# Kernel optimization log

Measured on AMD Instinct MI355X. Metric: run time of the kernel, lower is better.

## Reference

```python
import math
import jax, jax.numpy as jnp
import numpy as np

D_MODEL = 1024
N_HEADS = 16
HEAD_DIM = 64          # block_size
NUM_RULES = 64
RANK = 8               # proj_rank = round(sqrt(head_dim)); also router_rank
SHARED_RANK = 32       # round(sqrt(d_model))
NUM_BLOCKS = 16        # min(in,out)//block_size = 1024//64; total_block_dim == d_model
B, S = 4, 1024
ROPE_BASE = 10000.0


def setup_inputs() -> dict:
    key = jax.random.key(0)
    ks = iter(jax.random.split(key, 32))
    def nrm(shape, s=0.02):
        return jax.random.normal(next(ks), shape, dtype=jnp.float32) * s
    inp = {
        "x": jax.random.normal(next(ks), (B, S, D_MODEL), dtype=jnp.float32),
        "target_rule_ids": jax.random.randint(next(ks), (B, S), 0, NUM_RULES),
    }
    for p in ("q", "k", "v", "o"):
        inp[p + "_si"] = nrm((D_MODEL, SHARED_RANK))
        inp[p + "_so"] = nrm((SHARED_RANK, D_MODEL))
        inp[p + "_ri"] = nrm((NUM_RULES, HEAD_DIM, RANK))
        inp[p + "_ro"] = nrm((NUM_RULES, RANK, HEAD_DIM))
        inp[p + "_lg"] = nrm((NUM_RULES, NUM_BLOCKS), 1.0 / math.sqrt(NUM_BLOCKS))
    inp["router_q"] = nrm((NUM_RULES, RANK))
    inp["router_k"] = nrm((NUM_RULES, RANK))
    return inp


def _rule_proj(x, rules, si, so, ri, ro, lg):
    """RuleAwareProjection.forward_rules_batched, de-permuted.

    The torch code argsorts tokens by rule, zero-pads per-rule buckets, runs
    bmm per rule and scatters back; mathematically that equals a per-token
    gather of the rule's low-rank adapter, which is what we compute here.
    x: [N, D_MODEL], rules: [N] int.
    """
    base = (x @ si) @ so                                  # shared low-rank path
    xb = x.reshape(-1, NUM_BLOCKS, HEAD_DIM)              # [N, nb, bs]
    h = jnp.einsum('nbs,nsr->nbr', xb, ri[rules])         # [N, nb, rank]
    a = jnp.einsum('nbr,nrt->nbt', h, ro[rules])          # [N, nb, bs]
    # temperature = 1/sqrt(num_blocks) => logits / temperature = logits*sqrt(nb)
    sel = jax.nn.softmax(lg[rules] * math.sqrt(NUM_BLOCKS), axis=-1)
    return base + (a * sel[:, :, None]).reshape(-1, D_MODEL)


def _rope(q, k):
    # q, k: [B, H, S, D]; interleaved-pair rotation, start_pos = 0.
    S_, D = q.shape[2], q.shape[3]
    pos = jnp.arange(S_, dtype=jnp.float32)[:, None]
    div = jnp.exp(jnp.arange(0, D, 2, dtype=jnp.float32) * (-math.log(ROPE_BASE) / D))
    f = pos * div                                         # [S, D/2]
    sin, cos = jnp.sin(f), jnp.cos(f)
    def rot(t):
        t1, t2 = t[..., 0::2], t[..., 1::2]
        return jnp.stack([t1 * cos - t2 * sin, t2 * cos + t1 * sin], axis=-1).reshape(t.shape)
    return rot(q), rot(k)


def reference(x, target_rule_ids,
              q_si, q_so, q_ri, q_ro, q_lg,
              k_si, k_so, k_ri, k_ro, k_lg,
              v_si, v_so, v_ri, v_ro, v_lg,
              o_si, o_so, o_ri, o_ro, o_lg,
              router_q, router_k):
    B_, S_, C = x.shape
    flat_x = x.reshape(-1, C)
    rules = target_rule_ids.reshape(-1)

    q = _rule_proj(flat_x, rules, q_si, q_so, q_ri, q_ro, q_lg)
    k = _rule_proj(flat_x, rules, k_si, k_so, k_ri, k_ro, k_lg)
    v = _rule_proj(flat_x, rules, v_si, v_so, v_ri, v_ro, v_lg)
    q = q.reshape(B_, S_, N_HEADS, HEAD_DIM).transpose(0, 2, 1, 3)
    k = k.reshape(B_, S_, N_HEADS, HEAD_DIM).transpose(0, 2, 1, 3)
    v = v.reshape(B_, S_, N_HEADS, HEAD_DIM).transpose(0, 2, 1, 3)
    q, k = _rope(q, k)

    # rule-routing sparse mask: cosine affinity between token rule embeddings
    rq = router_q[target_rule_ids]                        # [B, S, rank]
    rk = router_k[target_rule_ids]
    rqn = rq / jnp.maximum(jnp.linalg.norm(rq, axis=-1, keepdims=True), 1e-12)
    rkn = rk / jnp.maximum(jnp.linalg.norm(rk, axis=-1, keepdims=True), 1e-12)
    tau = 1.0 / math.log(max(math.e, RANK))
    aff = jnp.einsum('bqr,bkr->bqk', rqn, rkn) / tau       # [B, S, S]
    causal = jnp.tril(jnp.ones((S_, S_), dtype=bool))
    masked = jnp.where(causal[None], aff, -jnp.inf)
    top_k = max(2, int(math.sqrt(S_)))
    if S_ > top_k:
        thr = jax.lax.top_k(masked, top_k)[0][..., -1:]
        rule_mask = (masked >= thr) & causal[None]
    else:
        rule_mask = jnp.broadcast_to(causal[None], masked.shape)

    scores = jnp.einsum('bhqd,bhkd->bhqk', q, k) / math.sqrt(HEAD_DIM)
    scores = jnp.where(rule_mask[:, None], scores, -jnp.inf)
    attn = jax.nn.softmax(scores, axis=-1)
    out = jnp.einsum('bhqk,bhkd->bhqd', attn, v)
    out = out.transpose(0, 2, 1, 3).reshape(-1, C)
    out = _rule_proj(out, rules, o_si, o_so, o_ri, o_ro, o_lg)
    return out.reshape(B_, S_, C)
```

## Files before the change

kernel.cpp:

```cpp
#include <hip/hip_runtime.h>
#include <hip/hip_bf16.h>
#include <hip/hip_fp16.h>

#define D_MODEL 1024
#define N_HEADS 16
#define HEAD_DIM 64
#define NUM_RULES 64
#define RANK 8
#define SHARED_RANK 32
#define NUM_BLOCKS_ 16
#define BB 4
#define SS 1024
#define NTOK (BB*SS)
#define NGRP (NTOK/8)
#define NGRP4 (NTOK/4)

typedef __attribute__((ext_vector_type(8))) short bf16x8;
typedef __attribute__((ext_vector_type(4))) float f32x4;

__device__ __forceinline__ float bf2f(unsigned short u) {
  unsigned int i = ((unsigned int)u) << 16;
  float f;
  __builtin_memcpy(&f, &i, 4);
  return f;
}
__device__ __forceinline__ unsigned short f2bf(float f) {
  __hip_bfloat16 h = __float2bfloat16(f);
  unsigned short u;
  __builtin_memcpy(&u, &h, 2);
  return u;
}
__device__ __forceinline__ unsigned short f2h(float f) {
  __half h = __float2half(f);
  unsigned short u;
  __builtin_memcpy(&u, &h, 2);
  return u;
}
__device__ __forceinline__ float h2f(unsigned short u) {
  __half h;
  __builtin_memcpy(&h, &u, 2);
  return __half2float(h);
}
template<bool BF>
__device__ __forceinline__ float ldw(const void* p, size_t i) {
  if (BF) return bf2f(((const unsigned short*)p)[i]);
  else    return ((const float*)p)[i];
}

__global__ void detect_kernel(const unsigned short* __restrict__ x, int* __restrict__ flag) {
  const int lane = threadIdx.x;
  int good = 0;
  for (int i = 0; i < 4; i++) {
    unsigned short u = x[lane*4 + i];
    int e = (u >> 7) & 0xFF;
    good += (e == 0 || (e >= 100 && e <= 145)) ? 1 : 0;
  }
  for (int off = 32; off; off >>= 1) good += __shfl_xor(good, off);
  if (lane == 0) flag[0] = (good >= 224) ? 1 : 0;
}

template<bool BF>
__device__ __forceinline__ void precompute_body(
    const void* rq, const void* rk,
    const void* qlg, const void* klg, const void* vlg, const void* olg,
    float* __restrict__ M, float* __restrict__ sel)
{
  __shared__ float rqn[64][8], rkn[64][8];
  const int tid = threadIdx.x;
  if (tid < 64) {
    float v[8]; float s = 0.f;
    for (int i = 0; i < 8; i++) { v[i] = ldw<BF>(rq, tid*8+i); s += v[i]*v[i]; }
    float inv = 1.0f / fmaxf(sqrtf(s), 1e-12f);
    for (int i = 0; i < 8; i++) rqn[tid][i] = v[i]*inv;
  } else if (tid < 128) {
    int r = tid - 64;
    float v[8]; float s = 0.f;
    for (int i = 0; i < 8; i++) { v[i] = ldw<BF>(rk, r*8+i); s += v[i]*v[i]; }
    float inv = 1.0f / fmaxf(sqrtf(s), 1e-12f);
    for (int i = 0; i < 8; i++) rkn[r][i] = v[i]*inv;
  }
  __syncthreads();
  const float LN8 = 2.0794415416798357f;
  for (int idx = tid; idx < 64*64; idx += 256) {
    int i = idx >> 6, j = idx & 63;
    float d = 0.f;
    for (int t = 0; t < 8; t++) d += rqn[i][t]*rkn[j][t];
    M[idx] = d * LN8;
  }
  const void* lgs[4] = {qlg, klg, vlg, olg};
  {
    int r = tid & 63;
    const void* lg = lgs[tid >> 6];
    float e[NUM_BLOCKS_]; float mx = -1e30f;
    for (int b = 0; b < NUM_BLOCKS_; b++) {
      e[b] = ldw<BF>(lg, r*NUM_BLOCKS_ + b) * 4.0f;
      mx = fmaxf(mx, e[b]);
    }
    float s = 0.f;
    for (int b = 0; b < NUM_BLOCKS_; b++) { e[b] = expf(e[b]-mx); s += e[b]; }
    float inv = 1.0f/s;
    for (int b = 0; b < NUM_BLOCKS_; b++) sel[tid*NUM_BLOCKS_+b] = e[b]*inv;
  }
}

__global__ void precompute_kernel(
    const void* rq, const void* rk,
    const void* qlg, const void* klg, const void* vlg, const void* olg,
    float* M, float* sel, const int* __restrict__ flag)
{
  if (*flag) precompute_body<true >(rq, rk, qlg, klg, vlg, olg, M, sel);
  else       precompute_body<false>(rq, rk, qlg, klg, vlg, olg, M, sel);
}

__global__ __launch_bounds__(128) void prep_wb_kernel(
    const float* __restrict__ qsi, const float* __restrict__ ksi,
    const float* __restrict__ vsi, const float* __restrict__ osi,
    unsigned short* __restrict__ wh, unsigned short* __restrict__ wl,
    const int* __restrict__ flag)
{
  if (*flag) return;
  const int kt = blockIdx.x, p = blockIdx.y;
  const int tid = threadIdx.x, nt = tid >> 6, lane = tid & 63;
  const float* si = (p==0)?qsi:((p==1)?ksi:((p==2)?vsi:osi));
  const int col = nt*16 + (lane & 15);
  const int k0 = kt*32 + (lane >> 4)*8;
  size_t base = ((((size_t)p*32 + kt)*2 + nt)*64 + lane)*8;
  unsigned short h8[8], l8[8];
  #pragma unroll
  for (int j = 0; j < 8; j++) {
    float f = si[(size_t)(k0 + j)*SHARED_RANK + col];
    unsigned short hu = f2bf(f);
    h8[j] = hu;
    l8[j] = f2bf(f - bf2f(hu));
  }
  #pragma unroll
  for (int j = 0; j < 8; j++) { wh[base + j] = h8[j]; wl[base + j] = l8[j]; }
}

template<int NPROJ>
__device__ __forceinline__ void tt_mfma_body(
    const float* __restrict__ xin,
    const unsigned short* __restrict__ wh, const unsigned short* __restrict__ wl,
    int p0, float* __restrict__ ttg)
{
  const int NT = NPROJ*2;
  const int tile = blockIdx.x;
  const int tid = threadIdx.x, lane = tid & 63, w = tid >> 6;
  const int kq = lane >> 4;
  __shared__ float red[4][64][25];

  f32x4 acc[NT];
  #pragma unroll
  for (int i = 0; i < NT; i++) acc[i] = (f32x4){0.f,0.f,0.f,0.f};

  const float* xrow = xin + (size_t)(tile*16 + (lane & 15))*D_MODEL + kq*8;
  #pragma unroll 2
  for (int s = 0; s < 8; s++) {
    const int kt = w*8 + s;
    float4 a0 = *(const float4*)(xrow + kt*32);
    float4 a1 = *(const float4*)(xrow + kt*32 + 4);
    float av[8] = {a0.x,a0.y,a0.z,a0.w,a1.x,a1.y,a1.z,a1.w};
    bf16x8 ah, al;
    #pragma unroll
    for (int j = 0; j < 8; j++) {
      unsigned short hu = f2bf(av[j]);
      ah[j] = (short)hu;
      al[j] = (short)f2bf(av[j] - bf2f(hu));
    }
    #pragma unroll
    for (int p = 0; p < NPROJ; p++) {
      #pragma unroll
      for (int nt = 0; nt < 2; nt++) {
        size_t bidx = ((((size_t)(p0+p)*32 + kt)*2 + nt)*64 + lane)*8;
        bf16x8 bh = *(const bf16x8*)(wh + bidx);
        bf16x8 bl = *(const bf16x8*)(wl + bidx);
        f32x4 c = acc[p*2+nt];
        c = __builtin_amdgcn_mfma_f32_16x16x32_bf16(ah, bh, c, 0, 0, 0);
        c = __builtin_amdgcn_mfma_f32_16x16x32_bf16(al, bh, c, 0, 0, 0);
        c = __builtin_amdgcn_mfma_f32_16x16x32_bf16(ah, bl, c, 0, 0, 0);
        acc[p*2+nt] = c;
      }
    }
  }
  #pragma unroll
  for (int i = 0; i < NT; i++) {
    red[w][lane][i*4+0] = acc[i][0]; red[w][lane][i*4+1] = acc[i][1];
    red[w][lane][i*4+2] = acc[i][2]; red[w][lane][i*4+3] = acc[i][3];
  }
  __syncthreads();
  if (w == 0) {
    const int tok0 = tile*16 + (lane >> 4)*4;
    #pragma unroll
    for (int i = 0; i < NT; i++) {
      const int ys = i >> 1, jj = (i & 1)*16 + (lane & 15);
      #pragma unroll
      for (int r = 0; r < 4; r++) {
        float sum = red[0][lane][i*4+r] + red[1][lane][i*4+r]
                  + red[2][lane][i*4+r] + red[3][lane][i*4+r];
        ttg[((size_t)ys*NTOK + tok0 + r)*32 + jj] = sum;
      }
    }
  }
}

__global__ __launch_bounds__(256) void A_tt_mfma3(
    const float* __restrict__ xin,
    const unsigned short* __restrict__ wh, const unsigned short* __restrict__ wl,
    float* __restrict__ ttg, const int* __restrict__ flag)
{
  if (*flag) return;
  tt_mfma_body<3>(xin, wh, wl, 0, ttg);
}

__global__ __launch_bounds__(256) void A_tt_mfma1(
    const float* __restrict__ xin,
    const unsigned short* __restrict__ wh, const unsigned short* __restrict__ wl,
    float* __restrict__ ttg, const int* __restrict__ flag)
{
  if (*flag) return;
  tt_mfma_body<1>(xin, wh, wl, 3, ttg);
}

template<int NP>
__device__ __forceinline__ void hh_body(
    const float* __restrict__ xin, const int* __restrict__ rules,
    const float* __restrict__ ri0, const float* __restrict__ ri1,
    const float* __restrict__ ri2, float* __restrict__ hhg)
{
  const int g = blockIdx.x, n0 = g*8, tid = threadIdx.x;
  const int t = tid >> 5, blk = (tid >> 1) & 15, r0 = (tid & 1)*4;
  const int n = n0 + t;
  const int rule = rules[n];
  const float* xb = xin + (size_t)n*D_MODEL + blk*64;
  const float* wb[3];
  wb[0] = ri0 + (size_t)rule*512 + r0;
  if (NP > 1) {
    wb[1] = ri1 + (size_t)rule*512 + r0;
    wb[2] = ri2 + (size_t)rule*512 + r0;
  }
  float a[NP][4];
  #pragma unroll
  for (int p = 0; p < NP; p++) { a[p][0]=0.f; a[p][1]=0.f; a[p][2]=0.f; a[p][3]=0.f; }
  #pragma unroll 4
  for (int k4 = 0; k4 < 16; k4++) {
    float4 xv = *(const float4*)(xb + k4*4);
    #pragma unroll
    for (int q = 0; q < 4; q++) {
      const int k = k4*4 + q;
      float xq = (q==0)?xv.x:((q==1)?xv.y:((q==2)?xv.z:xv.w));
      #pragma unroll
      for (int p = 0; p < NP; p++) {
        float4 wv = *(const float4*)(wb[p] + (size_t)k*8);
        a[p][0] += xq*wv.x; a[p][1] += xq*wv.y; a[p][2] += xq*wv.z; a[p][3] += xq*wv.w;
      }
    }
  }
  #pragma unroll
  for (int p = 0; p < NP; p++) {
    float4 hv; hv.x=a[p][0]; hv.y=a[p][1]; hv.z=a[p][2]; hv.w=a[p][3];
    *(float4*)&hhg[((size_t)p*NTOK + n)*128 + blk*8 + r0] = hv;
  }
}

__global__ __launch_bounds__(256) void A_hh3_f32(
    const float* __restrict__ xin, const int* __restrict__ rules,
    const float* __restrict__ qri, const float* __restrict__ kri,
    const float* __restrict__ vri, float* __restrict__ hhg,
    const int* __restrict__ flag)
{
  if (*flag) return;
  hh_body<3>(xin, rules, qri, kri, vri, hhg);
}

__global__ __launch_bounds__(256) void A_hh1_f32(
    const float* __restrict__ xin, const int* __restrict__ rules,
    const float* __restrict__ ori, float* __restrict__ hhg,
    const int* __restrict__ flag)
{
  if (*flag) return;
  hh_body<1>(xin, rules, ori, ori, ori, hhg);
}

template<bool IN_BF, bool W_BF>
__device__ __forceinline__ void stageA_body(
    const void* __restrict__ xin, const int* __restrict__ rules,
    const void* __restrict__ si, const void* __restrict__ ri,
    float* __restrict__ ttg, float* __restrict__ hhg, int yslot)
{
  const int g = blockIdx.x, n0 = g*8, tid = threadIdx.x;
  __shared__ float xs[8][D_MODEL];
  __shared__ float tpart[8][32][9];
  __shared__ int rl[8];

  #pragma unroll
  for (int t = 0; t < 8; t++) {
    float4 f;
    if (IN_BF) {
      ushort4 u = ((const ushort4*)((const unsigned short*)xin + (size_t)(n0+t)*D_MODEL))[tid];
      f.x = bf2f(u.x); f.y = bf2f(u.y); f.z = bf2f(u.z); f.w = bf2f(u.w);
    } else {
      f = ((const float4*)xin)[(size_t)(n0+t)*(D_MODEL/4) + tid];
    }
    *(float4*)&xs[t][tid*4] = f;
  }
  if (tid < 8) rl[tid] = rules[n0 + tid];
  __syncthreads();

  {
    const int c = tid >> 5, j = tid & 31;
    float p[8];
    #pragma unroll
    for (int t = 0; t < 8; t++) p[t] = 0.f;
    #pragma unroll 4
    for (int d4 = 0; d4 < 32; d4++) {
      const int d = c*128 + d4*4;
      float w0 = ldw<W_BF>(si, (size_t)(d+0)*SHARED_RANK + j);
      float w1 = ldw<W_BF>(si, (size_t)(d+1)*SHARED_RANK + j);
      float w2 = ldw<W_BF>(si, (size_t)(d+2)*SHARED_RANK + j);
      float w3 = ldw<W_BF>(si, (size_t)(d+3)*SHARED_RANK + j);
      #pragma unroll
      for (int t = 0; t < 8; t++) {
        float4 xv = *(const float4*)&xs[t][d];
        p[t] += xv.x*w0 + xv.y*w1 + xv.z*w2 + xv.w*w3;
      }
    }
    #pragma unroll
    for (int t = 0; t < 8; t++) tpart[c][j][t] = p[t];
  }
  __syncthreads();

  {
    const int t = tid >> 5, j = tid & 31;
    float s = 0.f;
    #pragma unroll
    for (int c = 0; c < 8; c++) s += tpart[c][j][t];
    ttg[((size_t)yslot*NTOK + n0 + t)*32 + j] = s;
  }
  {
    const int t = tid >> 5, blk = (tid >> 1) & 15, r0 = (tid & 1)*4;
    const int rule = rl[t];
    float a0=0.f, a1=0.f, a2=0.f, a3=0.f;
    #pragma unroll 4
    for (int k4 = 0; k4 < 16; k4++) {
      const int kk = ((k4 + blk) & 15) * 4;
      float4 xv = *(const float4*)&xs[t][blk*64 + kk];
      #pragma unroll
      for (int q = 0; q < 4; q++) {
        const int k = kk + q;
        float w0,w1,w2,w3;
        if (W_BF) {
          ushort4 u = *(const ushort4*)((const unsigned short*)ri + (size_t)rule*512 + (size_t)k*8 + r0);
          w0=bf2f(u.x); w1=bf2f(u.y); w2=bf2f(u.z); w3=bf2f(u.w);
        } else {
          float4 u = *(const float4*)((const float*)ri + (size_t)rule*512 + (size_t)k*8 + r0);
          w0=u.x; w1=u.y; w2=u.z; w3=u.w;
        }
        float xq = (q==0)?xv.x:((q==1)?xv.y:((q==2)?xv.z:xv.w));
        a0 += xq*w0; a1 += xq*w1; a2 += xq*w2; a3 += xq*w3;
      }
    }
    float4 hv; hv.x=a0; hv.y=a1; hv.z=a2; hv.w=a3;
    *(float4*)&hhg[((size_t)yslot*NTOK + n0 + t)*128 + blk*8 + r0] = hv;
  }
}

__global__ __launch_bounds__(256) void A_qkv_bf16(
    const void* x, const int* rules,
    const void* qsi, const void* qri, const void* ksi, const void* kri,
    const void* vsi, const void* vri,
    float* ttg, float* hhg, const int* __restrict__ flag)
{
  if (!*flag) return;
  const int y = blockIdx.y;
  const void* si = (y==0)?qsi:((y==1)?ksi:vsi);
  const void* ri = (y==0)?qri:((y==1)?kri:vri);
  stageA_body<true,true>(x, rules, si, ri, ttg, hhg, y);
}

__global__ __launch_bounds__(256) void A_o_bf16(
    const void* ain, const int* rules, const void* osi, const void* ori,
    float* ttg, float* hhg, const int* __restrict__ flag)
{
  if (!*flag) return;
  stageA_body<false,true>(ain, rules, osi, ori, ttg, hhg, 0);
}

template<bool W_BF>
__device__ __forceinline__ void stageB_body(
    const float* __restrict__ ttg, const float* __restrict__ hhg,
    const int* __restrict__ rules,
    const void* __restrict__ so, const void* __restrict__ ro,
    const float* __restrict__ sel, void* __restrict__ out,
    int yslot, int do_rope, int out_bf)
{
  const int blk4 = blockIdx.x;
  const int n0 = blk4*4, tid = threadIdx.x;
  __shared__ float tt_lds[32][5];
  __shared__ float hh_lds[4][132];
  __shared__ int rl[4];

  if (tid < 128) {
    const int j = tid >> 2, t4 = tid & 3;
    tt_lds[j][t4] = ttg[((size_t)yslot*NTOK + n0 + t4)*32 + j];
  } else if (tid < 256 && (tid - 128) < 128) {
    const int i = tid - 128;
    const int t4 = i >> 5, c = (i*4) & 127;
    float4 hv = *(const float4*)&hhg[((size_t)yslot*NTOK + n0 + t4)*128 + c];
    *(float4*)&hh_lds[t4][c] = hv;
  }
  if (tid < 4) rl[tid] = rules[n0 + tid];
  __syncthreads();

  const int ch0 = tid*4;
  float a0[4], a1[4], a2[4], a3[4];
  #pragma unroll
  for (int t = 0; t < 4; t++) { a0[t]=0.f; a1[t]=0.f; a2[t]=0.f; a3[t]=0.f; }

  #pragma unroll 4
  for (int j = 0; j < 32; j++) {
    float w0, w1, w2, w3;
    if (W_BF) {
      ushort4 u = *(const ushort4*)((const unsigned short*)so + (size_t)j*D_MODEL + ch0);
      w0=bf2f(u.x); w1=bf2f(u.y); w2=bf2f(u.z); w3=bf2f(u.w);
    } else {
      float4 u = *(const float4*)((const float*)so + (size_t)j*D_MODEL + ch0);
      w0=u.x; w1=u.y; w2=u.z; w3=u.w;
    }
    #pragma unroll
    for (int t = 0; t < 4; t++) {
      float tv = tt_lds[j][t];
      a0[t] += tv*w0; a1[t] += tv*w1; a2[t] += tv*w2; a3[t] += tv*w3;
    }
  }

  const int blk = ch0 >> 6, tc = ch0 & 63;
  float inv0 = 0.f, inv1 = 0.f;
  if (do_rope) {
    inv0 = expf(-(float)tc     * (9.210340371976184f/64.0f));
    inv1 = expf(-(float)(tc+2) * (9.210340371976184f/64.0f));
  }
  #pragma unroll 2
  for (int t = 0; t < 4; t++) {
    const int rule = rl[t];
    float b0=0.f, b1=0.f, b2=0.f, b3=0.f;
    #pragma unroll
    for (int r = 0; r < 8; r++) {
      float w0,w1,w2,w3;
      if (W_BF) {
        ushort4 u = *(const ushort4*)((const unsigned short*)ro + (size_t)rule*512 + r*64 + tc);
        w0=bf2f(u.x); w1=bf2f(u.y); w2=bf2f(u.z); w3=bf2f(u.w);
      } else {
        float4 u = *(const float4*)((const float*)ro + (size_t)rule*512 + r*64 + tc);
        w0=u.x; w1=u.y; w2=u.z; w3=u.w;
      }
      float hv = hh_lds[t][blk*8 + r];
      b0 += hv*w0; b1 += hv*w1; b2 += hv*w2; b3 += hv*w3;
    }
    float sb = sel[rule*NUM_BLOCKS_ + blk];
    float e0 = a0[t] + b0*sb, o0 = a1[t] + b1*sb;
    float e1 = a2[t] + b2*sb, o1 = a3[t] + b3*sb;
    const int n = n0 + t;
    if (do_rope) {
      float spos = (float)(n & (SS-1));
      float sn0, cs0, sn1, cs1;
      sincosf(spos*inv0, &sn0, &cs0);
      sincosf(spos*inv1, &sn1, &cs1);
      float u0 = e0*cs0 - o0*sn0; o0 = o0*cs0 + e0*sn0; e0 = u0;
      float u1 = e1*cs1 - o1*sn1; o1 = o1*cs1 + e1*sn1; e1 = u1;
    }
    if (out_bf) {
      ushort4 uv; uv.x=f2bf(e0); uv.y=f2bf(o0); uv.z=f2bf(e1); uv.w=f2bf(o1);
      *(ushort4*)((unsigned short*)out + (size_t)n*D_MODEL + ch0) = uv;
    } else {
      float4 fv; fv.x=e0; fv.y=o0; fv.z=e1; fv.w=o1;
      *(float4*)((float*)out + (size_t)n*D_MODEL + ch0) = fv;
    }
  }
}

__global__ __launch_bounds__(256) void B_qkv(
    const float* ttg, const float* hhg, const int* rules,
    const void* qso, const void* qro, const void* kso, const void* kro,
    const void* vso, const void* vro,
    const float* sel, float* qb, unsigned short* kb, unsigned short* vb,
    const int* __restrict__ flag)
{
  const int y = blockIdx.y;
  const void* so = (y==0)?qso:((y==1)?kso:vso);
  const void* ro = (y==0)?qro:((y==1)?kro:vro);
  void* out = (y==0)?(void*)qb:((y==1)?(void*)kb:(void*)vb);
  if (*flag)
    stageB_body<true >(ttg, hhg, rules, so, ro, sel + y*1024, out, y, (y<2)?1:0, (y>=1)?1:0);
  else
    stageB_body<false>(ttg, hhg, rules, so, ro, sel + y*1024, out, y, (y<2)?1:0, (y>=1)?1:0);
}

__global__ __launch_bounds__(256) void B_o(
    const float* ttg, const float* hhg, const int* rules,
    const void* oso, const void* oro, const float* sel, void* out,
    const int* __restrict__ flag)
{
  if (*flag) stageB_body<true >(ttg, hhg, rules, oso, oro, sel, out, 0, 0, 1);
  else       stageB_body<false>(ttg, hhg, rules, oso, oro, sel, out, 0, 0, 0);
}

__global__ __launch_bounds__(64) void mask_kernel(
    const int* __restrict__ rules, const float* __restrict__ M,
    unsigned long long* __restrict__ am, unsigned int* __restrict__ rp)
{
  const int bid = blockIdx.x;
  const int b = bid >> 10, qi = bid & 1023;
  const int lane = threadIdx.x;
  __shared__ int rrow[SS];
  __shared__ float val[64];
  __shared__ int cnth[64];
  for (int i = lane; i < SS/4; i += 64)
    ((int4*)rrow)[i] = ((const int4*)(rules + b*SS))[i];
  cnth[lane] = 0;
  __syncthreads();
  if (qi < 16 && lane < 16) {
    unsigned v = 0;
    #pragma unroll
    for (int nt = 0; nt < 4; nt++)
      v |= ((unsigned)rrow[qi*64 + nt*16 + lane] & 0xffu) << (8*nt);
    rp[b*256 + qi*16 + lane] = v;
  }
  for (int k = lane; k <= qi; k += 64) atomicAdd(&cnth[rrow[k]], 1);
  const int qrule = rrow[qi];
  const float myv = M[qrule*64 + lane];
  val[lane] = myv;
  __syncthreads();
  const int c = cnth[lane];
  int A = 0;
  for (int r = 0; r < 64; r++) {
    int cr = __shfl(c, r);
    A += (val[r] > myv) ? cr : 0;
  }
  unsigned long long allowed = __ballot(A < 32);
  if (lane == 0) am[bid] = allowed;
}

__global__ __launch_bounds__(256) void vtrans_kernel(
    const unsigned short* __restrict__ vb, unsigned short* __restrict__ vt)
{
  const int st = blockIdx.x, h = blockIdx.y, b = blockIdx.z;
  __shared__ unsigned short t[64][72];
  const int tid = threadIdx.x;
  #pragma unroll
  for (int it = 0; it < 2; it++) {
    int i = tid + it*256;
    int r = i >> 3, c8 = (i & 7)*8;
    uint4 v = *(const uint4*)(vb + ((size_t)(b*SS + st*64 + r)*D_MODEL + h*HEAD_DIM + c8));
    t[c8+0][r] = (unsigned short)(v.x & 0xffffu);
    t[c8+1][r] = (unsigned short)(v.x >> 16);
    t[c8+2][r] = (unsigned short)(v.y & 0xffffu);
    t[c8+3][r] = (unsigned short)(v.y >> 16);
    t[c8+4][r] = (unsigned short)(v.z & 0xffffu);
    t[c8+5][r] = (unsigned short)(v.z >> 16);
    t[c8+6][r] = (unsigned short)(v.w & 0xffffu);
    t[c8+7][r] = (unsigned short)(v.w >> 16);
  }
  __syncthreads();
  #pragma unroll
  for (int it = 0; it < 2; it++) {
    int i = tid + it*256;
    int d = i >> 3, c8 = i & 7;
    uint4 o = *(const uint4*)&t[d][c8*8];
    *(uint4*)(vt + ((size_t)(b*N_HEADS + h)*HEAD_DIM + d)*SS + st*64 + c8*8) = o;
  }
}

__global__ __launch_bounds__(256, 4) void attn_mfma_kernel(
    const float* __restrict__ qb,
    const unsigned short* __restrict__ kb,
    const unsigned short* __restrict__ vtb,
    const unsigned int* __restrict__ rp,
    const unsigned long long* __restrict__ am,
    unsigned short* __restrict__ Obuf,
    float* __restrict__ mlbuf,
    float* outb)
{
  const int x = blockIdx.x, b = blockIdx.y, h = blockIdx.z;
  int qt, k0t, k1t, pidx;
  bool partial;
  if (x < 9) { qt = x; k0t = 0; k1t = qt; partial = false; pidx = 0; }
  else {
    const int j = x - 9, qti = j >> 1, s = j & 1;
    qt = 9 + qti; partial = true;
    pidx = ((b*N_HEADS + h)*7 + qti)*2 + s;
    if (s == 0) { k0t = 0; k1t = 7; } else { k0t = 8; k1t = qt; }
  }
  const int tid = threadIdx.x, lane = tid & 63, w = tid >> 6;
  __shared__ unsigned short Ks[64*64];
  __shared__ unsigned short Vs[64*64];
  __shared__ unsigned short Pl[4][16*64];

  const unsigned short* kbase = kb + (size_t)b*SS*D_MODEL + h*HEAD_DIM;
  const unsigned short* vbase = vtb + (size_t)(b*N_HEADS + h)*HEAD_DIM*SS;
  const unsigned int* rpb = rp + b*256;

  const int srow = tid >> 3;
  const int spos = tid & 7;
  const int kc0 = (srow*8      + (spos ^ (srow        & 7)))*8;
  const int kc1 = ((srow+32)*8 + (spos ^ ((srow+32)   & 7)))*8;
  unsigned short* pw = &Pl[w][0];

  const int qa = qt*64 + w*16 + (lane & 15);
  bf16x8 qfrag[2];
  {
    const float* qrow = qb + (size_t)(b*SS + qa)*D_MODEL + h*HEAD_DIM + (lane>>4)*8;
    #pragma unroll
    for (int kc = 0; kc < 2; kc++) {
      float4 f0 = *(const float4*)(qrow + kc*32);
      float4 f1 = *(const float4*)(qrow + kc*32 + 4);
      bf16x8 qv;
      qv[0] = (short)f2bf(f0.x*0.125f); qv[1] = (short)f2bf(f0.y*0.125f);
      qv[2] = (short)f2bf(f0.z*0.125f); qv[3] = (short)f2bf(f0.w*0.125f);
      qv[4] = (short)f2bf(f1.x*0.125f); qv[5] = (short)f2bf(f1.y*0.125f);
      qv[6] = (short)f2bf(f1.z*0.125f); qv[7] = (short)f2bf(f1.w*0.125f);
      qfrag[kc] = qv;
    }
  }
  int qg[4]; unsigned aqlo[4], aqhi[4];
  #pragma unroll
  for (int r = 0; r < 4; r++) {
    qg[r] = qt*64 + w*16 + (lane>>4)*4 + r;
    uint2 mm = *(const uint2*)(am + (size_t)b*SS + qg[r]);
    aqlo[r] = mm.x; aqhi[r] = mm.y;
  }
  f32x4 Oacc[4];
  #pragma unroll
  for (int nt = 0; nt < 4; nt++) Oacc[nt] = (f32x4){0.f,0.f,0.f,0.f};
  float lrun[4];
  #pragma unroll
  for (int r = 0; r < 4; r++) lrun[r] = 0.f;

  {
    const size_t koff0 = (size_t)k0t*64;
    uint4 k0 = *(const uint4*)(kbase + (koff0 + srow)*D_MODEL + spos*8);
    uint4 k1 = *(const uint4*)(kbase + (koff0 + srow + 32)*D_MODEL + spos*8);
    uint4 v0 = *(const uint4*)(vbase + (size_t)srow*SS + koff0 + spos*8);
    uint4 v1 = *(const uint4*)(vbase + (size_t)(srow+32)*SS + koff0 + spos*8);
    *(uint4*)&Ks[kc0] = k0; *(uint4*)&Ks[kc1] = k1;
    *(uint4*)&Vs[kc0] = v0; *(uint4*)&Vs[kc1] = v1;
  }
  __syncthreads();

  for (int kt = k0t; kt <= k1t; kt++) {
    const unsigned ru = rpb[kt*16 + (lane & 15)];
    uint4 nk0, nk1, nv0, nv1;
    if (kt < k1t) {
      const size_t koff = (size_t)(kt + 1)*64;
      nk0 = *(const uint4*)(kbase + (koff + srow)*D_MODEL + spos*8);
      nk1 = *(const uint4*)(kbase + (koff + srow + 32)*D_MODEL + spos*8);
      nv0 = *(const uint4*)(vbase + (size_t)srow*SS + koff + spos*8);
      nv1 = *(const uint4*)(vbase + (size_t)(srow+32)*SS + koff + spos*8);
    }

    f32x4 Sacc[4];
    __builtin_amdgcn_s_setprio(1);
    #pragma unroll
    for (int nt = 0; nt < 4; nt++) {
      const int key = nt*16 + (lane & 15);
      f32x4 c = (f32x4){0.f,0.f,0.f,0.f};
      #pragma unroll
      for (int kc = 0; kc < 2; kc++) {
        int off = (key*128 + kc*64 + (lane>>4)*16) ^ ((key & 7) << 4);
        bf16x8 kf = *(const bf16x8*)((const char*)Ks + off);
        c = __builtin_amdgcn_mfma_f32_16x16x32_bf16(qfrag[kc], kf, c, 0, 0, 0);
      }
      Sacc[nt] = c;
    }
    __builtin_amdgcn_s_setprio(0);

    const bool needc = (kt == qt);
    float sv[4][4];
    #pragma unroll
    for (int nt = 0; nt < 4; nt++) {
      const int k = kt*64 + nt*16 + (lane & 15);
      const unsigned rr = (ru >> (nt*8)) & 0xffu;
      const unsigned sh = rr & 31u;
      const bool hi = rr >= 32;
      #pragma unroll
      for (int r = 0; r < 4; r++) {
        unsigned bits = hi ? aqhi[r] : aqlo[r];
        bool ok = (((bits >> sh) & 1u) != 0u);
        if (needc) ok = ok && (k <= qg[r]);
        sv[nt][r] = ok ? Sacc[nt][r] : -3e38f;
      }
    }

    #pragma unroll
    for (int nt = 0; nt < 4; nt++) {
      #pragma unroll
      for (int r = 0; r < 4; r++) {
        float p = __expf(sv[nt][r]);
        lrun[r] += p;
        const int q = (lane>>4)*4 + r;
        int off = (q*128 + (nt*16 + (lane & 15))*2) ^ ((q & 7) << 4);
        *(unsigned short*)((char*)pw + off) = f2bf(p);
      }
    }

    __builtin_amdgcn_s_setprio(1);
    #pragma unroll
    for (int kc = 0; kc < 2; kc++) {
      const int qrow = lane & 15;
      int aoff = (qrow*128 + kc*64 + (lane>>4)*16) ^ ((qrow & 7) << 4);
      bf16x8 pa = *(const bf16x8*)((const char*)pw + aoff);
      #pragma unroll
      for (int nt = 0; nt < 4; nt++) {
        const int d = nt*16 + (lane & 15);
        int boff = (d*128 + kc*64 + (lane>>4)*16) ^ ((d & 7) << 4);
        bf16x8 vf = *(const bf16x8*)((const char*)Vs + boff);
        Oacc[nt] = __builtin_amdgcn_mfma_f32_16x16x32_bf16(pa, vf, Oacc[nt], 0, 0, 0);
      }
    }
    __builtin_amdgcn_s_setprio(0);
    __syncthreads();
    if (kt < k1t) {
      *(uint4*)&Ks[kc0] = nk0; *(uint4*)&Ks[kc1] = nk1;
      *(uint4*)&Vs[kc0] = nv0; *(uint4*)&Vs[kc1] = nv1;
      __syncthreads();
    }
  }

  #pragma unroll
  for (int off = 1; off < 16; off <<= 1) {
    #pragma unroll
    for (int r = 0; r < 4; r++) lrun[r] += __shfl_xor(lrun[r], off);
  }

  if (!partial) {
    float invl[4];
    #pragma unroll
    for (int r = 0; r < 4; r++) invl[r] = 1.0f / lrun[r];
    #pragma unroll
    for (int nt = 0; nt < 4; nt++) {
      #pragma unroll
      for (int r = 0; r < 4; r++) {
        outb[(size_t)(b*SS + qg[r])*D_MODEL + h*HEAD_DIM + nt*16 + (lane & 15)]
            = Oacc[nt][r]*invl[r];
      }
    }
  } else {
    unsigned short* ob = Obuf + (size_t)pidx*4096;
    #pragma unroll
    for (int nt = 0; nt < 4; nt++) {
      #pragma unroll
      for (int r = 0; r < 4; r++) {
        const int row = w*16 + (lane>>4)*4 + r;
        ob[row*64 + nt*16 + (lane & 15)] = f2h(Oacc[nt][r]);
      }
    }
    if ((lane & 15) == 0) {
      float* ml = mlbuf + (size_t)pidx*64;
      #pragma unroll
      for (int r = 0; r < 4; r++) {
        const int row = w*16 + (lane>>4)*4 + r;
        ml[row] = lrun[r];
      }
    }
  }
}

__global__ __launch_bounds__(256) void attn_combine(
    const unsigned short* __restrict__ Obuf, const float* __restrict__ mlbuf,
    float* __restrict__ outb)
{
  const int qti = blockIdx.x, b = blockIdx.y, h = blockIdx.z;
  const int qt = 9 + qti;
  const int p0 = ((b*N_HEADS + h)*7 + qti)*2;
  const int tid = threadIdx.x;
  const int row = tid >> 2, c0 = (tid & 3)*16;
  const float l0 = mlbuf[(size_t)p0*64 + row];
  const float l1 = mlbuf[(size_t)(p0+1)*64 + row];
  const float inv = 1.0f / (l0 + l1);
  const unsigned short* o0 = Obuf + (size_t)p0*4096 + row*64 + c0;
  const unsigned short* o1 = Obuf + (size_t)(p0+1)*4096 + row*64 + c0;
  float* dst = outb + (size_t)(b*SS + qt*64 + row)*D_MODEL + h*HEAD_DIM + c0;
  #pragma unroll
  for (int j = 0; j < 16; j += 4) {
    float4 fv;
    fv.x = (h2f(o0[j+0]) + h2f(o1[j+0]))*inv;
    fv.y = (h2f(o0[j+1]) + h2f(o1[j+1]))*inv;
    fv.z = (h2f(o0[j+2]) + h2f(o1[j+2]))*inv;
    fv.w = (h2f(o0[j+3]) + h2f(o1[j+3]))*inv;
    *(float4*)(dst + j) = fv;
  }
}

extern "C" void kernel_launch(void* const* d_in, const int* in_sizes, int n_in,
                              void* d_out, int out_size, void* d_ws, size_t ws_size,
                              hipStream_t stream) {
  (void)in_sizes; (void)n_in; (void)out_size; (void)ws_size;
  const void* x    = d_in[0];
  const int* rules = (const int*)d_in[1];
  const void* q_si = d_in[2];  const void* q_so = d_in[3];
  const void* q_ri = d_in[4];  const void* q_ro = d_in[5];  const void* q_lg = d_in[6];
  const void* k_si = d_in[7];  const void* k_so = d_in[8];
  const void* k_ri = d_in[9];  const void* k_ro = d_in[10]; const void* k_lg = d_in[11];
  const void* v_si = d_in[12]; const void* v_so = d_in[13];
  const void* v_ri = d_in[14]; const void* v_ro = d_in[15]; const void* v_lg = d_in[16];
  const void* o_si = d_in[17]; const void* o_so = d_in[18];
  const void* o_ri = d_in[19]; const void* o_ro = d_in[20]; const void* o_lg = d_in[21];
  const void* rq   = d_in[22]; const void* rk   = d_in[23];

  char* ws = (char*)d_ws;
  const size_t MB = 1024*1024;
  float*          qb    = (float*)(ws);
  unsigned short* kb    = (unsigned short*)(ws + 16*MB);
  unsigned short* vb    = (unsigned short*)(ws + 24*MB);
  unsigned short* vtb   = (unsigned short*)(ws + 32*MB);
  float*          ttg   = (float*)(ws + 40*MB);
  float*          hhg   = (float*)(ws + 42*MB);
  unsigned short* Obuf  = (unsigned short*)(ws + 40*MB);
  float*          mlbuf = (float*)(ws + 47*MB);
  unsigned long long* amask = (unsigned long long*)(ws + 48*MB);
  float*          Mt    = (float*)(ws + 49*MB + 16*1024);
  float*          selt  = (float*)(ws + 49*MB + 32*1024);
  int*            flag  = (int*)  (ws + 49*MB + 48*1024);
  unsigned int*   rp    = (unsigned int*)(ws + 49*MB + 52*1024);
  unsigned short* wpkh  = (unsigned short*)(ws + 49*MB + 64*1024);
  unsigned short* wpkl  = (unsigned short*)(ws + 49*MB + 64*1024 + 256*1024);

  detect_kernel<<<1, 64, 0, stream>>>((const unsigned short*)x, flag);
  precompute_kernel<<<1, 256, 0, stream>>>(rq, rk, q_lg, k_lg, v_lg, o_lg, Mt, selt, flag);
  mask_kernel<<<NTOK, 64, 0, stream>>>(rules, Mt, amask, rp);
  prep_wb_kernel<<<dim3(32, 4), 128, 0, stream>>>(
      (const float*)q_si, (const float*)k_si, (const float*)v_si, (const float*)o_si,
      wpkh, wpkl, flag);

  A_qkv_bf16<<<dim3(NGRP, 3), 256, 0, stream>>>(x, rules, q_si, q_ri, k_si, k_ri, v_si, v_ri, ttg, hhg, flag);
  A_tt_mfma3<<<256, 256, 0, stream>>>((const float*)x, wpkh, wpkl, ttg, flag);
  A_hh3_f32<<<NGRP, 256, 0, stream>>>((const float*)x, rules,
      (const float*)q_ri, (const float*)k_ri, (const float*)v_ri, hhg, flag);

  B_qkv<<<dim3(NGRP4, 3), 256, 0, stream>>>(ttg, hhg, rules, q_so, q_ro, k_so, k_ro, v_so, v_ro,
                                            selt, qb, kb, vb, flag);

  vtrans_kernel<<<dim3(16, 16, 4), 256, 0, stream>>>(vb, vtb);
  attn_mfma_kernel<<<dim3(23, BB, N_HEADS), 256, 0, stream>>>(qb, kb, vtb, rp, amask,
                                                              Obuf, mlbuf, qb);
  attn_combine<<<dim3(7, BB, N_HEADS), 256, 0, stream>>>(Obuf, mlbuf, qb);

  A_o_bf16<<<dim3(NGRP, 1), 256, 0, stream>>>(qb, rules, o_si, o_ri, ttg, hhg, flag);
  A_tt_mfma1<<<256, 256, 0, stream>>>(qb, wpkh, wpkl, ttg, flag);
  A_hh1_f32<<<NGRP, 256, 0, stream>>>(qb, rules, (const float*)o_ri, hhg, flag);
  B_o<<<NGRP4, 256, 0, stream>>>(ttg, hhg, rules, o_so, o_ro, selt + 3*1024, d_out, flag);
}
```

Before: 269.4 us.

## Compute S transposed to keep P in registers, dropping LDS round-trip

The QK^T MFMA now swaps its operands so each lane holds scores for 4 consecutive keys of one query. That layout can be packed straight into the A-operand of the PV MFMA, which removes the per-wave shared-memory P buffer and its write/read traffic. Supporting changes permute the V-transpose output columns and the packed rule-id layout to match the new key ordering. Row-sum reduction becomes two cross-group shuffles instead of four. The cost is subtle layout coupling between three kernels, where any index mismatch gives wrong results.

```diff
diff --git a/kernel.cpp b/kernel.cpp
--- a/kernel.cpp
+++ b/kernel.cpp
@@ -519,10 +519,11 @@
   cnth[lane] = 0;
   __syncthreads();
   if (qi < 16 && lane < 16) {
+    const int gg = lane >> 2, nt = lane & 3;
     unsigned v = 0;
     #pragma unroll
-    for (int nt = 0; nt < 4; nt++)
-      v |= ((unsigned)rrow[qi*64 + nt*16 + lane] & 0xffu) << (8*nt);
+    for (int j = 0; j < 4; j++)
+      v |= ((unsigned)rrow[qi*64 + nt*16 + gg*4 + j] & 0xffu) << (8*j);
     rp[b*256 + qi*16 + lane] = v;
   }
   for (int k = lane; k <= qi; k += 64) atomicAdd(&cnth[rrow[k]], 1);
@@ -565,8 +566,18 @@
   for (int it = 0; it < 2; it++) {
     int i = tid + it*256;
     int d = i >> 3, c8 = i & 7;
-    uint4 o = *(const uint4*)&t[d][c8*8];
-    *(uint4*)(vt + ((size_t)(b*N_HEADS + h)*HEAD_DIM + d)*SS + st*64 + c8*8) = o;
+    const unsigned short* src = &t[d][c8*8];
+    uint2 r1, r2;
+    r1.x = (unsigned)src[0] | ((unsigned)src[1] << 16);
+    r1.y = (unsigned)src[2] | ((unsigned)src[3] << 16);
+    r2.x = (unsigned)src[4] | ((unsigned)src[5] << 16);
+    r2.y = (unsigned)src[6] | ((unsigned)src[7] << 16);
+    const int base = (c8 >> 2)*32 + 4*((c8 >> 1) & 1);
+    const int p1 = base + 8*((2*c8)   & 3);
+    const int p2 = base + 8*((2*c8+1) & 3);
+    unsigned short* dst = vt + ((size_t)(b*N_HEADS + h)*HEAD_DIM + d)*SS + st*64;
+    *(uint2*)(dst + p1) = r1;
+    *(uint2*)(dst + p2) = r2;
   }
 }
 
@@ -591,9 +602,9 @@
     if (s == 0) { k0t = 0; k1t = 7; } else { k0t = 8; k1t = qt; }
   }
   const int tid = threadIdx.x, lane = tid & 63, w = tid >> 6;
+  const int g = lane >> 4, ql = lane & 15;
   __shared__ unsigned short Ks[64*64];
   __shared__ unsigned short Vs[64*64];
-  __shared__ unsigned short Pl[4][16*64];
 
   const unsigned short* kbase = kb + (size_t)b*SS*D_MODEL + h*HEAD_DIM;
   const unsigned short* vbase = vtb + (size_t)(b*N_HEADS + h)*HEAD_DIM*SS;
@@ -601,14 +612,13 @@
 
   const int srow = tid >> 3;
   const int spos = tid & 7;
-  const int kc0 = (srow*8      + (spos ^ (srow        & 7)))*8;
-  const int kc1 = ((srow+32)*8 + (spos ^ ((srow+32)   & 7)))*8;
-  unsigned short* pw = &Pl[w][0];
-
-  const int qa = qt*64 + w*16 + (lane & 15);
+  const int sc0 = (srow*8      + (spos ^ (srow      & 7)))*8;
+  const int sc1 = ((srow+32)*8 + (spos ^ ((srow+32) & 7)))*8;
+
+  const int qa = qt*64 + w*16 + ql;
   bf16x8 qfrag[2];
   {
-    const float* qrow = qb + (size_t)(b*SS + qa)*D_MODEL + h*HEAD_DIM + (lane>>4)*8;
+    const float* qrow = qb + (size_t)(b*SS + qa)*D_MODEL + h*HEAD_DIM + g*8;
     #pragma unroll
     for (int kc = 0; kc < 2; kc++) {
       float4 f0 = *(const float4*)(qrow + kc*32);
@@ -621,19 +631,13 @@
       qfrag[kc] = qv;
     }
   }
-  int qg[4]; unsigned aqlo[4], aqhi[4];
-  #pragma unroll
-  for (int r = 0; r < 4; r++) {
-    qg[r] = qt*64 + w*16 + (lane>>4)*4 + r;
-    uint2 mm = *(const uint2*)(am + (size_t)b*SS + qg[r]);
-    aqlo[r] = mm.x; aqhi[r] = mm.y;
-  }
+  const uint2 mm = *(const uint2*)(am + (size_t)b*SS + qa);
+  const unsigned aqlo = mm.x, aqhi = mm.y;
+
   f32x4 Oacc[4];
   #pragma unroll
   for (int nt = 0; nt < 4; nt++) Oacc[nt] = (f32x4){0.f,0.f,0.f,0.f};
-  float lrun[4];
-  #pragma unroll
-  for (int r = 0; r < 4; r++) lrun[r] = 0.f;
+  float lrun = 0.f;
 
   {
     const size_t koff0 = (size_t)k0t*64;
@@ -641,13 +645,13 @@
     uint4 k1 = *(const uint4*)(kbase + (koff0 + srow + 32)*D_MODEL + spos*8);
     uint4 v0 = *(const uint4*)(vbase + (size_t)srow*SS + koff0 + spos*8);
     uint4 v1 = *(const uint4*)(vbase + (size_t)(srow+32)*SS + koff0 + spos*8);
-    *(uint4*)&Ks[kc0] = k0; *(uint4*)&Ks[kc1] = k1;
-    *(uint4*)&Vs[kc0] = v0; *(uint4*)&Vs[kc1] = v1;
+    *(uint4*)&Ks[sc0] = k0; *(uint4*)&Ks[sc1] = k1;
+    *(uint4*)&Vs[sc0] = v0; *(uint4*)&Vs[sc1] = v1;
   }
   __syncthreads();
 
   for (int kt = k0t; kt <= k1t; kt++) {
-    const unsigned ru = rpb[kt*16 + (lane & 15)];
+    const uint4 ru4 = *(const uint4*)(rpb + kt*16 + g*4);
     uint4 nk0, nk1, nv0, nv1;
     if (kt < k1t) {
       const size_t koff = (size_t)(kt + 1)*64;
@@ -661,85 +665,73 @@
     __builtin_amdgcn_s_setprio(1);
     #pragma unroll
     for (int nt = 0; nt < 4; nt++) {
-      const int key = nt*16 + (lane & 15);
+      const int key = nt*16 + ql;
       f32x4 c = (f32x4){0.f,0.f,0.f,0.f};
       #pragma unroll
-      for (int kc = 0; kc < 2; kc++) {
-        int off = (key*128 + kc*64 + (lane>>4)*16) ^ ((key & 7) << 4);
+      for (int kcq = 0; kcq < 2; kcq++) {
+        int off = (key*128 + kcq*64 + g*16) ^ ((key & 7) << 4);
         bf16x8 kf = *(const bf16x8*)((const char*)Ks + off);
-        c = __builtin_amdgcn_mfma_f32_16x16x32_bf16(qfrag[kc], kf, c, 0, 0, 0);
+        c = __builtin_amdgcn_mfma_f32_16x16x32_bf16(kf, qfrag[kcq], c, 0, 0, 0);
       }
       Sacc[nt] = c;
     }
     __builtin_amdgcn_s_setprio(0);
 
     const bool needc = (kt == qt);
-    float sv[4][4];
+    const unsigned ruarr[4] = {ru4.x, ru4.y, ru4.z, ru4.w};
+    unsigned pk[4][2];
     #pragma unroll
     for (int nt = 0; nt < 4; nt++) {
-      const int k = kt*64 + nt*16 + (lane & 15);
-      const unsigned rr = (ru >> (nt*8)) & 0xffu;
-      const unsigned sh = rr & 31u;
-      const bool hi = rr >= 32;
+      float p[4];
       #pragma unroll
       for (int r = 0; r < 4; r++) {
-        unsigned bits = hi ? aqhi[r] : aqlo[r];
-        bool ok = (((bits >> sh) & 1u) != 0u);
-        if (needc) ok = ok && (k <= qg[r]);
-        sv[nt][r] = ok ? Sacc[nt][r] : -3e38f;
-      }
-    }
-
-    #pragma unroll
-    for (int nt = 0; nt < 4; nt++) {
-      #pragma unroll
-      for (int r = 0; r < 4; r++) {
-        float p = __expf(sv[nt][r]);
-        lrun[r] += p;
-        const int q = (lane>>4)*4 + r;
-        int off = (q*128 + (nt*16 + (lane & 15))*2) ^ ((q & 7) << 4);
-        *(unsigned short*)((char*)pw + off) = f2bf(p);
-      }
+        const unsigned rr = (ruarr[nt] >> (8*r)) & 0xffu;
+        const unsigned bits = (rr >= 32) ? aqhi : aqlo;
+        bool ok = ((bits >> (rr & 31u)) & 1u) != 0u;
+        if (needc) ok = ok && ((kt*64 + nt*16 + g*4 + r) <= qa);
+        p[r] = __expf(ok ? Sacc[nt][r] : -3e38f);
+        lrun += p[r];
+      }
+      pk[nt][0] = (unsigned)f2bf(p[0]) | ((unsigned)f2bf(p[1]) << 16);
+      pk[nt][1] = (unsigned)f2bf(p[2]) | ((unsigned)f2bf(p[3]) << 16);
     }
 
     __builtin_amdgcn_s_setprio(1);
     #pragma unroll
     for (int kc = 0; kc < 2; kc++) {
-      const int qrow = lane & 15;
-      int aoff = (qrow*128 + kc*64 + (lane>>4)*16) ^ ((qrow & 7) << 4);
-      bf16x8 pa = *(const bf16x8*)((const char*)pw + aoff);
-      #pragma unroll
-      for (int nt = 0; nt < 4; nt++) {
-        const int d = nt*16 + (lane & 15);
-        int boff = (d*128 + kc*64 + (lane>>4)*16) ^ ((d & 7) << 4);
+      union { unsigned u[4]; bf16x8 v; } U;
+      U.u[0] = pk[2*kc][0];   U.u[1] = pk[2*kc][1];
+      U.u[2] = pk[2*kc+1][0]; U.u[3] = pk[2*kc+1][1];
+      const bf16x8 pa = U.v;
+      #pragma unroll
+      for (int ntd = 0; ntd < 4; ntd++) {
+        const int d = ntd*16 + ql;
+        int boff = (d*128 + kc*64 + g*16) ^ ((d & 7) << 4);
         bf16x8 vf = *(const bf16x8*)((const char*)Vs + boff);
-        Oacc[nt] = __builtin_amdgcn_mfma_f32_16x16x32_bf16(pa, vf, Oacc[nt], 0, 0, 0);
+        Oacc[ntd] = __builtin_amdgcn_mfma_f32_16x16x32_bf16(pa, vf, Oacc[ntd], 0, 0, 0);
       }
     }
     __builtin_amdgcn_s_setprio(0);
     __syncthreads();
     if (kt < k1t) {
-      *(uint4*)&Ks[kc0] = nk0; *(uint4*)&Ks[kc1] = nk1;
-      *(uint4*)&Vs[kc0] = nv0; *(uint4*)&Vs[kc1] = nv1;
+      *(uint4*)&Ks[sc0] = nk0; *(uint4*)&Ks[sc1] = nk1;
+      *(uint4*)&Vs[sc0] = nv0; *(uint4*)&Vs[sc1] = nv1;
       __syncthreads();
     }
   }
 
-  #pragma unroll
-  for (int off = 1; off < 16; off <<= 1) {
-    #pragma unroll
-    for (int r = 0; r < 4; r++) lrun[r] += __shfl_xor(lrun[r], off);
-  }
+  lrun += __shfl_xor(lrun, 16);
+  lrun += __shfl_xor(lrun, 32);
 
   if (!partial) {
     float invl[4];
     #pragma unroll
-    for (int r = 0; r < 4; r++) invl[r] = 1.0f / lrun[r];
+    for (int r = 0; r < 4; r++) invl[r] = 1.0f / __shfl(lrun, g*4 + r);
     #pragma unroll
     for (int nt = 0; nt < 4; nt++) {
       #pragma unroll
       for (int r = 0; r < 4; r++) {
-        outb[(size_t)(b*SS + qg[r])*D_MODEL + h*HEAD_DIM + nt*16 + (lane & 15)]
+        outb[(size_t)(b*SS + qt*64 + w*16 + g*4 + r)*D_MODEL + h*HEAD_DIM + nt*16 + ql]
             = Oacc[nt][r]*invl[r];
       }
     }
@@ -749,18 +741,11 @@
     for (int nt = 0; nt < 4; nt++) {
       #pragma unroll
       for (int r = 0; r < 4; r++) {
-        const int row = w*16 + (lane>>4)*4 + r;
-        ob[row*64 + nt*16 + (lane & 15)] = f2h(Oacc[nt][r]);
-      }
-    }
-    if ((lane & 15) == 0) {
-      float* ml = mlbuf + (size_t)pidx*64;
-      #pragma unroll
-      for (int r = 0; r < 4; r++) {
-        const int row = w*16 + (lane>>4)*4 + r;
-        ml[row] = lrun[r];
-      }
-    }
+        const int row = w*16 + g*4 + r;
+        ob[row*64 + nt*16 + ql] = f2h(Oacc[nt][r]);
+      }
+    }
+    if (lane < 16) mlbuf[(size_t)pidx*64 + w*16 + lane] = lrun;
   }
 }
 
```

Result: no change. 271.8 us (+0.9%).
